# Performance work log

Hardware: AMD Instinct MI355X
Metric: run time of the kernel (lower is better)

The kernel has to match this reference:

```python
import jax, jax.numpy as jnp
import numpy as np

B, T, D, U = 64, 1024, 300, 300


def setup_inputs() -> dict:
    key = jax.random.key(0)
    ks = jax.random.split(key, 12)
    inputs = jax.random.normal(ks[0], (B, T, D), jnp.float32)
    lengths = jax.random.randint(ks[1], (B,), T // 2, T + 1)
    mask = jnp.arange(T)[None, :] < lengths[:, None]  # [B,T] bool

    def w(k, shape, fan_in):
        return jax.random.normal(k, shape, jnp.float32) * (1.0 / np.sqrt(fan_in))

    # Keras GRU (reset_after=True): kernel [D,3U], recurrent_kernel [U,3U], bias [2,3U]
    k_fwd = w(ks[2], (D, 3 * U), D)
    rk_fwd = w(ks[3], (U, 3 * U), U)
    b_fwd = jnp.zeros((2, 3 * U), jnp.float32)
    k_bwd = w(ks[4], (D, 3 * U), D)
    rk_bwd = w(ks[5], (U, 3 * U), U)
    b_bwd = jnp.zeros((2, 3 * U), jnp.float32)
    w_fc = w(ks[6], (2 * U, U), 2 * U)
    b_fc = jnp.zeros((U,), jnp.float32)
    return {
        "inputs": inputs, "mask": mask,
        "k_fwd": k_fwd, "rk_fwd": rk_fwd, "b_fwd": b_fwd,
        "k_bwd": k_bwd, "rk_bwd": rk_bwd, "b_bwd": b_bwd,
        "w_fc": w_fc, "b_fc": b_fc, "training": 0,
    }


def _gru_dir(x, mask, kernel, rkernel, bias):
    """Keras GRU v2 (reset_after=True), zero_output_for_mask, state frozen on masked steps.
    x: [B,T,D], mask: [B,T] bool -> (ys [B,T,U], h_final [B,U])"""
    b_in, b_rec = bias[0], bias[1]
    u = rkernel.shape[0]
    # precompute input projections for all timesteps (cuDNN-style hoisting)
    xp = jnp.einsum('btd,dk->btk', x, kernel) + b_in  # [B,T,3U]

    def step(h, inp):
        xt, mt = inp  # xt: [B,3U], mt: [B]
        rp = h @ rkernel + b_rec  # [B,3U]
        xz, xr, xh = jnp.split(xt, 3, axis=-1)
        rz, rr, rh = jnp.split(rp, 3, axis=-1)
        z = jax.nn.sigmoid(xz + rz)
        r = jax.nn.sigmoid(xr + rr)
        hh = jnp.tanh(xh + r * rh)
        h_new = z * h + (1.0 - z) * hh
        m = mt[:, None]
        h_carry = jnp.where(m, h_new, h)       # state does not update on masked steps
        y = jnp.where(m, h_new, jnp.zeros_like(h_new))  # zero_output_for_mask
        return h_carry, y

    h0 = jnp.zeros((x.shape[0], u), x.dtype)
    h_final, ys = jax.lax.scan(step, h0, (xp.transpose(1, 0, 2), mask.T))
    return ys.transpose(1, 0, 2), h_final


def reference(inputs, mask, k_fwd, rk_fwd, b_fwd, k_bwd, rk_bwd, b_bwd, w_fc, b_fc, training):
    mask = mask.astype(bool)
    x = inputs  # Dropout is identity at inference (training=0)
    y_f, h_f = _gru_dir(x, mask, k_fwd, rk_fwd, b_fwd)
    # backward direction: process reversed sequence/mask, then re-reverse outputs
    y_b, h_b = _gru_dir(x[:, ::-1], mask[:, ::-1], k_bwd, rk_bwd, b_bwd)
    y_b = y_b[:, ::-1]
    output = jnp.concatenate([y_f, y_b], axis=-1)  # [B,T,2U]
    state = jax.nn.relu(jnp.concatenate([h_f, h_b], axis=-1) @ w_fc + b_fc)  # [B,U]
    return output, state
```

## Files before the change

### kernel.cpp

```cpp
#include <hip/hip_runtime.h>
#include <hip/hip_bf16.h>


#define B_   64
#define T_   1024
#define D_   300
#define U_   300
#define NU   900
#define KP   320
#define NP   960
#define XPW  912
#define KL   32

typedef short short8 __attribute__((ext_vector_type(8)));
typedef float floatx4 __attribute__((ext_vector_type(4)));

__device__ __forceinline__ float b2f_bits(unsigned short u) {
  union { unsigned int i; float f; } v; v.i = ((unsigned int)u) << 16; return v.f;
}
__device__ __forceinline__ float lo16(unsigned int w) {
  union { unsigned int i; float f; } v; v.i = w << 16; return v.f;
}
__device__ __forceinline__ float hi16(unsigned int w) {
  union { unsigned int i; float f; } v; v.i = w & 0xffff0000u; return v.f;
}
__device__ __forceinline__ unsigned short f2b(float f) {
  __hip_bfloat16 h = __float2bfloat16(f);
  return *reinterpret_cast<unsigned short*>(&h);
}

__global__ __launch_bounds__(64) void k_detect(const unsigned int* __restrict__ xw,
                                               const unsigned char* __restrict__ mb,
                                               int* __restrict__ flags) {
  __shared__ int red[64];
  int tid = threadIdx.x;
  int hits = 0;
  for (int i = tid; i < 2048; i += 64) {
    unsigned int lo = xw[i] & 0xFFFFu;
    int e = (int)((lo >> 7) & 0xFF);
    if (e >= 105 && e <= 135) hits++;
  }
  red[tid] = hits;
  __syncthreads();
  if (tid == 0) {
    int s = 0;
    for (int i = 0; i < 64; ++i) s += red[i];
    flags[0] = (s >= 1024) ? 1 : 0;
    unsigned char b0 = mb[0], b1 = mb[1];
    flags[1] = (b1 == 0) ? 0 : ((b0 == 1 && b1 == 1) ? 1 : 2);
  }
}

__global__ __launch_bounds__(256) void k_lengths(const unsigned char* __restrict__ mraw,
                                                 const int* __restrict__ flags,
                                                 int* __restrict__ lens) {
  __shared__ int red[256];
  int b = blockIdx.x, tid = threadIdx.x;
  int mt = flags[1];
  int s = 0;
  if (mt == 0) {
    const int* m = (const int*)mraw;
    for (int t = tid; t < T_; t += 256) s += m[(size_t)b * T_ + t] ? 1 : 0;
  } else if (mt == 1) {
    for (int t = tid; t < T_; t += 256) s += mraw[(size_t)b * T_ + t] ? 1 : 0;
  } else {
    const unsigned short* m = (const unsigned short*)mraw;
    for (int t = tid; t < T_; t += 256) s += m[(size_t)b * T_ + t] ? 1 : 0;
  }
  red[tid] = s; __syncthreads();
  for (int off = 128; off > 0; off >>= 1) {
    if (tid < off) red[tid] += red[tid + off];
    __syncthreads();
  }
  if (tid == 0) lens[b] = red[0];
}

__global__ __launch_bounds__(256) void k_xpad(const void* __restrict__ xraw,
                                              const int* __restrict__ flags,
                                              unsigned short* __restrict__ xp) {
  int id = blockIdx.x * 256 + threadIdx.x;
  int row = id / 40, seg = id % 40;
  int kbase = seg * 8;
  int bf = flags[0];
  unsigned short v[8];
  if (bf) {
    const unsigned short* x = (const unsigned short*)xraw;
#pragma unroll
    for (int i = 0; i < 8; ++i) {
      int k = kbase + i;
      v[i] = (k < D_) ? x[(size_t)row * D_ + k] : (unsigned short)0;
    }
  } else {
    const float* x = (const float*)xraw;
#pragma unroll
    for (int i = 0; i < 8; ++i) {
      int k = kbase + i;
      v[i] = (k < D_) ? f2b(x[(size_t)row * D_ + k]) : (unsigned short)0;
    }
  }
  uint4 o;
  o.x = (unsigned)v[0] | ((unsigned)v[1] << 16);
  o.y = (unsigned)v[2] | ((unsigned)v[3] << 16);
  o.z = (unsigned)v[4] | ((unsigned)v[5] << 16);
  o.w = (unsigned)v[6] | ((unsigned)v[7] << 16);
  *(uint4*)(xp + (size_t)row * KP + kbase) = o;
}

__global__ __launch_bounds__(256) void k_wpad(const void* __restrict__ kf,
                                              const void* __restrict__ kb,
                                              const int* __restrict__ flags,
                                              unsigned short* __restrict__ kp) {
  int id = blockIdx.x * 256 + threadIdx.x;
  if (id >= 2 * KP * NP) return;
  int dir = id / (KP * NP);
  int r = id % (KP * NP);
  int k = r / NP, n = r % NP;
  int bf = flags[0];
  unsigned short v = 0;
  if (k < D_ && n < NU) {
    size_t si = (size_t)k * NU + n;
    if (bf) v = ((const unsigned short*)(dir ? kb : kf))[si];
    else    v = f2b(((const float*)(dir ? kb : kf))[si]);
  }
  kp[id] = v;
}

__global__ __launch_bounds__(256) void k_prep(const void* __restrict__ rkf,
                                              const void* __restrict__ rkb,
                                              const void* __restrict__ bfw,
                                              const void* __restrict__ bbw,
                                              const void* __restrict__ wfc,
                                              const void* __restrict__ bfc,
                                              const int* __restrict__ flags,
                                              unsigned short* __restrict__ rkc,
                                              float* __restrict__ biasc,
                                              unsigned short* __restrict__ wfcc,
                                              float* __restrict__ bfcc) {
  int i = blockIdx.x * 256 + threadIdx.x;
  int bf = flags[0];
  if (i < 2 * D_ * NU) {
    int dir = i / (D_ * NU), r = i % (D_ * NU);
    const void* src = dir ? rkb : rkf;
    rkc[i] = bf ? ((const unsigned short*)src)[r] : f2b(((const float*)src)[r]);
  }
  if (i < 2 * 2 * NU) {
    int dir = i / (2 * NU), r = i % (2 * NU);
    const void* src = dir ? bbw : bfw;
    biasc[i] = bf ? b2f_bits(((const unsigned short*)src)[r]) : ((const float*)src)[r];
  }
  if (i < 2 * U_ * U_) {
    wfcc[i] = bf ? ((const unsigned short*)wfc)[i] : f2b(((const float*)wfc)[i]);
  }
  if (i < U_) {
    bfcc[i] = bf ? b2f_bits(((const unsigned short*)bfc)[i]) : ((const float*)bfc)[i];
  }
}

template <bool XPF32>
__global__ __launch_bounds__(256) void k_gemm(const unsigned short* __restrict__ xpad,
                                              const unsigned short* __restrict__ kpad,
                                              const float* __restrict__ biasc,
                                              void* __restrict__ xp_out) {
  __shared__ __align__(16) unsigned short As[64 * 40];
  __shared__ __align__(16) unsigned short Bs[64 * 40];
  int tid = threadIdx.x;
  int wave = tid >> 6, lane = tid & 63;
  int m0 = blockIdx.x * 64, n0 = blockIdx.y * 64;
  int dir = blockIdx.z;
  const unsigned short* Bsrc = kpad + (size_t)dir * KP * NP;
  const float* bin = biasc + (size_t)dir * 2 * NU;

  floatx4 acc[4];
#pragma unroll
  for (int i = 0; i < 4; ++i) acc[i] = {0.f, 0.f, 0.f, 0.f};

  int arow = tid >> 2, aseg = tid & 3;
  int bk = tid & 31, bn8 = (tid >> 5) * 8;
  int fr = lane & 15, fq = lane >> 4;

  for (int kc = 0; kc < KP; kc += 32) {
    uint4 av = *(const uint4*)(xpad + (size_t)(m0 + arow) * KP + kc + aseg * 8);
    uint4 bv = *(const uint4*)(Bsrc + (size_t)(kc + bk) * NP + n0 + bn8);
    *(uint4*)(As + arow * 40 + aseg * 8) = av;
    unsigned short tmp[8];
    tmp[0] = bv.x & 0xffff; tmp[1] = bv.x >> 16;
    tmp[2] = bv.y & 0xffff; tmp[3] = bv.y >> 16;
    tmp[4] = bv.z & 0xffff; tmp[5] = bv.z >> 16;
    tmp[6] = bv.w & 0xffff; tmp[7] = bv.w >> 16;
#pragma unroll
    for (int i = 0; i < 8; ++i) Bs[(bn8 + i) * 40 + bk] = tmp[i];
    __syncthreads();
    short8 a = *(const short8*)(As + (wave * 16 + fr) * 40 + fq * 8);
#pragma unroll
    for (int nt = 0; nt < 4; ++nt) {
      short8 bfrag = *(const short8*)(Bs + (nt * 16 + fr) * 40 + fq * 8);
      acc[nt] = __builtin_amdgcn_mfma_f32_16x16x32_bf16(a, bfrag, acc[nt], 0, 0, 0);
    }
    __syncthreads();
  }
#pragma unroll
  for (int nt = 0; nt < 4; ++nt) {
    int col = n0 + nt * 16 + fr;
    if (col >= XPW) continue;
    float bi = (col < NU) ? bin[col] : 0.f;
#pragma unroll
    for (int r = 0; r < 4; ++r) {
      int m = m0 + wave * 16 + fq * 4 + r;
      float v = acc[nt][r] + bi;
      size_t idx = ((size_t)dir * 65536 + m) * XPW + col;
      if (XPF32) ((float*)xp_out)[idx] = v;
      else ((unsigned short*)xp_out)[idx] = f2b(v);
    }
  }
}

template <bool XPF32>
__global__ __launch_bounds__(256) void k_scan(const unsigned short* __restrict__ rkc,
                                              const float* __restrict__ biasc,
                                              const void* __restrict__ xp_all,
                                              const int* __restrict__ lens,
                                              const int* __restrict__ flags,
                                              float* __restrict__ hfin,
                                              void* __restrict__ outraw)
{
  __shared__ __align__(16) unsigned short wlds[KL * NU];
  __shared__ __align__(16) float h[304];
  __shared__ __align__(16) float rp[912];
  int tid = threadIdx.x;
  int b = blockIdx.x, dir = blockIdx.y;
  const unsigned short* rk = rkc + (size_t)dir * D_ * NU;
  const float* brec = biasc + (size_t)dir * 2 * NU + NU;
  int len = lens[b];
  int obf = flags[0];
  unsigned short* out16 = (unsigned short*)outraw;
  float* out32 = (float*)outraw;

  {
    const unsigned int* src = (const unsigned int*)rk;
    unsigned int* dst = (unsigned int*)wlds;
    for (int i = tid; i < KL * NU / 2; i += 256) dst[i] = src[i];
  }
  for (int i = tid; i < 304; i += 256) h[i] = 0.f;
  __syncthreads();

  int c = tid;
  int j = 4 * c;

  for (int s = 0; s < T_; ++s) {
    int t = dir ? (T_ - 1 - s) : s;
    size_t row = (size_t)b * T_ + t;
    if (t < len) {
      if (c < 225) {
        float a0 = brec[j], a1 = brec[j + 1], a2 = brec[j + 2], a3 = brec[j + 3];
        for (int k0 = 0; k0 < KL; k0 += 4) {
          float4 h4 = *(const float4*)(h + k0);
#pragma unroll
          for (int i = 0; i < 4; ++i) {
            uint2 w = *(const uint2*)(wlds + (k0 + i) * NU + j);
            float hk = ((const float*)&h4)[i];
            a0 = fmaf(lo16(w.x), hk, a0);
            a1 = fmaf(hi16(w.x), hk, a1);
            a2 = fmaf(lo16(w.y), hk, a2);
            a3 = fmaf(hi16(w.y), hk, a3);
          }
        }
        for (int k0 = KL; k0 < D_; k0 += 4) {
          float4 h4 = *(const float4*)(h + k0);
#pragma unroll
          for (int i = 0; i < 4; ++i) {
            uint2 w = *(const uint2*)(rk + (size_t)(k0 + i) * NU + j);
            float hk = ((const float*)&h4)[i];
            a0 = fmaf(lo16(w.x), hk, a0);
            a1 = fmaf(hi16(w.x), hk, a1);
            a2 = fmaf(lo16(w.y), hk, a2);
            a3 = fmaf(hi16(w.y), hk, a3);
          }
        }
        rp[j] = a0; rp[j + 1] = a1; rp[j + 2] = a2; rp[j + 3] = a3;
      }
      __syncthreads();
      for (int u = tid; u < U_; u += 256) {
        float xz, xr, xh;
        if (XPF32) {
          const float* xrow = (const float*)xp_all + ((size_t)dir * 65536 + row) * XPW;
          xz = xrow[u]; xr = xrow[u + U_]; xh = xrow[u + 2 * U_];
        } else {
          const unsigned short* xrow =
              (const unsigned short*)xp_all + ((size_t)dir * 65536 + row) * XPW;
          xz = b2f_bits(xrow[u]); xr = b2f_bits(xrow[u + U_]); xh = b2f_bits(xrow[u + 2 * U_]);
        }
        float z = 1.f / (1.f + __expf(-(xz + rp[u])));
        float r = 1.f / (1.f + __expf(-(xr + rp[u + U_])));
        float hh = tanhf(xh + r * rp[u + 2 * U_]);
        float hold = h[u];
        float hn = z * hold + (1.f - z) * hh;
        h[u] = hn;
        size_t oi = row * 600 + (size_t)dir * U_ + u;
        if (obf) out16[oi] = f2b(hn); else out32[oi] = hn;
      }
      __syncthreads();
    } else {
      for (int u = tid; u < U_; u += 256) {
        size_t oi = row * 600 + (size_t)dir * U_ + u;
        if (obf) out16[oi] = 0; else out32[oi] = 0.f;
      }
    }
  }
  for (int u = tid; u < U_; u += 256) hfin[((size_t)dir * B_ + b) * 304 + u] = h[u];
}

__global__ __launch_bounds__(320) void k_state(const float* __restrict__ hfin,
                                               const unsigned short* __restrict__ wfcc,
                                               const float* __restrict__ bfcc,
                                               const int* __restrict__ flags,
                                               void* __restrict__ outraw) {
  int b = blockIdx.x, u = threadIdx.x;
  if (u >= U_) return;
  int obf = flags[0];
  float acc = bfcc[u];
  const float* hf = hfin + (size_t)b * 304;
  const float* hb = hfin + ((size_t)B_ + b) * 304;
  for (int k = 0; k < U_; ++k) acc = fmaf(hf[k], b2f_bits(wfcc[(size_t)k * U_ + u]), acc);
  for (int k = 0; k < U_; ++k) acc = fmaf(hb[k], b2f_bits(wfcc[(size_t)(U_ + k) * U_ + u]), acc);
  float v = fmaxf(acc, 0.f);
  size_t oi = (size_t)B_ * T_ * 600 + (size_t)b * U_ + u;
  if (obf) ((unsigned short*)outraw)[oi] = f2b(v);
  else     ((float*)outraw)[oi] = v;
}

extern "C" void kernel_launch(void* const* d_in, const int* in_sizes, int n_in,
                              void* d_out, int out_size, void* d_ws, size_t ws_size,
                              hipStream_t stream) {
  const void* x    = d_in[0];
  const void* mask = d_in[1];
  const void* kf   = d_in[2];
  const void* rkf  = d_in[3];
  const void* bfw  = d_in[4];
  const void* kb   = d_in[5];
  const void* rkb  = d_in[6];
  const void* bbw  = d_in[7];
  const void* wfc  = d_in[8];
  const void* bfc  = d_in[9];

  char* ws = (char*)d_ws;
  size_t off = 0;
  auto alloc = [&](size_t bytes) { void* p = ws + off; off += (bytes + 255) & ~(size_t)255; return p; };
  int* flags            = (int*)alloc(256);
  int* lens             = (int*)alloc(256);
  unsigned short* xpad  = (unsigned short*)alloc((size_t)65536 * KP * 2);
  unsigned short* kpad  = (unsigned short*)alloc((size_t)2 * KP * NP * 2);
  unsigned short* rkc   = (unsigned short*)alloc((size_t)2 * D_ * NU * 2);
  float* biasc          = (float*)alloc((size_t)2 * 2 * NU * 4);
  unsigned short* wfcc  = (unsigned short*)alloc((size_t)2 * U_ * U_ * 2);
  float* bfcc           = (float*)alloc((size_t)U_ * 4);
  float* hfin           = (float*)alloc((size_t)2 * B_ * 304 * 4);
  void* xp = (void*)(ws + off);
  size_t need_f32 = off + (size_t)2 * 65536 * XPW * 4;
  bool xpf32 = ws_size >= need_f32;

  k_detect<<<dim3(1), dim3(64), 0, stream>>>((const unsigned int*)x, (const unsigned char*)mask, flags);
  k_lengths<<<dim3(B_), dim3(256), 0, stream>>>((const unsigned char*)mask, flags, lens);
  k_xpad<<<dim3(65536 * 40 / 256), dim3(256), 0, stream>>>(x, flags, xpad);
  k_wpad<<<dim3((2 * KP * NP + 255) / 256), dim3(256), 0, stream>>>(kf, kb, flags, kpad);
  k_prep<<<dim3((2 * D_ * NU + 255) / 256), dim3(256), 0, stream>>>(rkf, rkb, bfw, bbw, wfc, bfc,
                                                                    flags, rkc, biasc, wfcc, bfcc);
  if (xpf32) {
    k_gemm<true><<<dim3(1024, 15, 2), dim3(256), 0, stream>>>(xpad, kpad, biasc, xp);
    k_scan<true><<<dim3(B_, 2), dim3(256), 0, stream>>>(rkc, biasc, xp, lens, flags, hfin, d_out);
  } else {
    k_gemm<false><<<dim3(1024, 15, 2), dim3(256), 0, stream>>>(xpad, kpad, biasc, xp);
    k_scan<false><<<dim3(B_, 2), dim3(256), 0, stream>>>(rkc, biasc, xp, lens, flags, hfin, d_out);
  }
  k_state<<<dim3(B_), dim3(320), 0, stream>>>(hfin, wfcc, bfcc, flags, d_out);
}
```

Before: 16.66 ms.

## Split GRU scan across workgroups by hidden units with MFMA and grid barrier

The recurrent scan used to give each batch row its own workgroup doing scalar bf16 FMAs over the full 300x900 recurrent matrix. Now 15 workgroups per direction each own 20 hidden units for all 64 batch rows. Each keeps its slice of the recurrent weights resident in registers and computes h@Rk with bf16 MFMA, using a hi/lo bf16 split of h to keep close to fp32 accuracy. Hidden state is exchanged through double-buffered global memory, with an atomic-counter grid barrier every timestep. This trades per-step global sync and spin-wait latency for far fewer redundant weight reads and use of the matrix cores. It relies on all 30 workgroups being co-resident.

```diff
diff --git a/kernel.cpp b/kernel.cpp
--- a/kernel.cpp
+++ b/kernel.cpp
@@ -10,19 +10,16 @@
 #define KP   320
 #define NP   960
 #define XPW  912
-#define KL   32
+#define NW   15
+#define W_   20
+#define HS   320
+#define KB_  10
 
 typedef short short8 __attribute__((ext_vector_type(8)));
 typedef float floatx4 __attribute__((ext_vector_type(4)));
 
 __device__ __forceinline__ float b2f_bits(unsigned short u) {
   union { unsigned int i; float f; } v; v.i = ((unsigned int)u) << 16; return v.f;
-}
-__device__ __forceinline__ float lo16(unsigned int w) {
-  union { unsigned int i; float f; } v; v.i = w << 16; return v.f;
-}
-__device__ __forceinline__ float hi16(unsigned int w) {
-  union { unsigned int i; float f; } v; v.i = w & 0xffff0000u; return v.f;
 }
 __device__ __forceinline__ unsigned short f2b(float f) {
   __hip_bfloat16 h = __float2bfloat16(f);
@@ -73,6 +70,17 @@
     __syncthreads();
   }
   if (tid == 0) lens[b] = red[0];
+}
+
+__global__ __launch_bounds__(256) void k_init(unsigned short* __restrict__ hHi,
+                                              unsigned short* __restrict__ hLo,
+                                              int* __restrict__ ctrs) {
+  int i = blockIdx.x * 256 + threadIdx.x;
+  const int nu = 2 * 2 * B_ * HS / 2;
+  unsigned int* a = (unsigned int*)hHi;
+  unsigned int* b = (unsigned int*)hLo;
+  if (i < nu) { a[i] = 0u; b[i] = 0u; }
+  if (i < 128) ctrs[i] = 0;
 }
 
 __global__ __launch_bounds__(256) void k_xpad(const void* __restrict__ xraw,
@@ -156,6 +164,30 @@
   }
 }
 
+__global__ __launch_bounds__(256) void k_bpack(const unsigned short* __restrict__ rkc,
+                                               unsigned short* __restrict__ bpack) {
+  int idx = blockIdx.x * 256 + threadIdx.x;
+  const int total = 2 * NW * 40 * 512;
+  if (idx >= total) return;
+  int rem = idx;
+  int j = rem & 7; rem >>= 3;
+  int lane = rem & 63; rem >>= 6;
+  int f = rem % 40; rem /= 40;
+  int wg = rem % NW;
+  int dir = rem / NW;
+  int kb = f >> 2, nt = f & 3;
+  int l15 = lane & 15, quad = lane >> 4;
+  int k = kb * 32 + quad * 8 + j;
+  int n = nt * 16 + l15;
+  unsigned short v = 0;
+  if (n < 3 * W_ && k < D_) {
+    int g = n / W_, i = n % W_;
+    int col = g * U_ + wg * W_ + i;
+    v = rkc[(size_t)dir * D_ * NU + (size_t)k * NU + col];
+  }
+  bpack[idx] = v;
+}
+
 template <bool XPF32>
 __global__ __launch_bounds__(256) void k_gemm(const unsigned short* __restrict__ xpad,
                                               const unsigned short* __restrict__ kpad,
@@ -215,98 +247,142 @@
 }
 
 template <bool XPF32>
-__global__ __launch_bounds__(256) void k_scan(const unsigned short* __restrict__ rkc,
-                                              const float* __restrict__ biasc,
-                                              const void* __restrict__ xp_all,
-                                              const int* __restrict__ lens,
-                                              const int* __restrict__ flags,
-                                              float* __restrict__ hfin,
-                                              void* __restrict__ outraw)
-{
-  __shared__ __align__(16) unsigned short wlds[KL * NU];
-  __shared__ __align__(16) float h[304];
-  __shared__ __align__(16) float rp[912];
+__global__ __launch_bounds__(256, 1) void k_scan(const unsigned short* __restrict__ bpack,
+                                                 const float* __restrict__ biasc,
+                                                 const void* __restrict__ xp_all,
+                                                 const int* __restrict__ lens,
+                                                 const int* __restrict__ flags,
+                                                 unsigned short* __restrict__ hHi,
+                                                 unsigned short* __restrict__ hLo,
+                                                 float* __restrict__ hfin,
+                                                 int* __restrict__ ctrs,
+                                                 void* __restrict__ outraw) {
+  __shared__ __align__(16) float rp[64 * 68];
   int tid = threadIdx.x;
-  int b = blockIdx.x, dir = blockIdx.y;
-  const unsigned short* rk = rkc + (size_t)dir * D_ * NU;
-  const float* brec = biasc + (size_t)dir * 2 * NU + NU;
-  int len = lens[b];
+  int wg = blockIdx.x, dir = blockIdx.y;
+  int wave = tid >> 6, lane = tid & 63;
+  int l15 = lane & 15, quad = lane >> 4;
   int obf = flags[0];
   unsigned short* out16 = (unsigned short*)outraw;
   float* out32 = (float*)outraw;
 
+  short8 breg[KB_][4];
   {
-    const unsigned int* src = (const unsigned int*)rk;
-    unsigned int* dst = (unsigned int*)wlds;
-    for (int i = tid; i < KL * NU / 2; i += 256) dst[i] = src[i];
-  }
-  for (int i = tid; i < 304; i += 256) h[i] = 0.f;
-  __syncthreads();
-
-  int c = tid;
-  int j = 4 * c;
-
+    const unsigned short* bp = bpack + ((size_t)(dir * NW + wg) * 40) * 512 + lane * 8;
+#pragma unroll
+    for (int kb = 0; kb < KB_; ++kb)
+#pragma unroll
+      for (int nt = 0; nt < 4; ++nt)
+        breg[kb][nt] = *(const short8*)(bp + (size_t)(kb * 4 + nt) * 512);
+  }
+
+  int eb = tid >> 2;
+  int ei = (tid & 3) * 5;
+  int u0 = wg * W_;
+  int mylen = lens[eb];
+  const float* brec = biasc + (size_t)dir * 2 * NU + NU;
+  float bz[5], brr[5], bh[5], hold[5];
+#pragma unroll
+  for (int q = 0; q < 5; ++q) {
+    int u = u0 + ei + q;
+    bz[q] = brec[u]; brr[q] = brec[U_ + u]; bh[q] = brec[2 * U_ + u];
+    hold[q] = 0.f;
+  }
+
+  int ctr_target = 0;
+  int* myctr = ctrs + dir * 64;
+
+#pragma unroll 1
   for (int s = 0; s < T_; ++s) {
     int t = dir ? (T_ - 1 - s) : s;
-    size_t row = (size_t)b * T_ + t;
-    if (t < len) {
-      if (c < 225) {
-        float a0 = brec[j], a1 = brec[j + 1], a2 = brec[j + 2], a3 = brec[j + 3];
-        for (int k0 = 0; k0 < KL; k0 += 4) {
-          float4 h4 = *(const float4*)(h + k0);
-#pragma unroll
-          for (int i = 0; i < 4; ++i) {
-            uint2 w = *(const uint2*)(wlds + (k0 + i) * NU + j);
-            float hk = ((const float*)&h4)[i];
-            a0 = fmaf(lo16(w.x), hk, a0);
-            a1 = fmaf(hi16(w.x), hk, a1);
-            a2 = fmaf(lo16(w.y), hk, a2);
-            a3 = fmaf(hi16(w.y), hk, a3);
-          }
+    int par = s & 1;
+    const unsigned short* hh = hHi + (size_t)(par * 2 + dir) * (B_ * HS);
+    const unsigned short* hl = hLo + (size_t)(par * 2 + dir) * (B_ * HS);
+
+    float xz[5], xr[5], xh[5];
+    {
+      size_t rowoff = ((size_t)dir * 65536 + (size_t)eb * T_ + t) * XPW;
+      if (XPF32) {
+        const float* xrow = (const float*)xp_all + rowoff;
+#pragma unroll
+        for (int q = 0; q < 5; ++q) {
+          int u = u0 + ei + q;
+          xz[q] = xrow[u]; xr[q] = xrow[U_ + u]; xh[q] = xrow[2 * U_ + u];
         }
-        for (int k0 = KL; k0 < D_; k0 += 4) {
-          float4 h4 = *(const float4*)(h + k0);
-#pragma unroll
-          for (int i = 0; i < 4; ++i) {
-            uint2 w = *(const uint2*)(rk + (size_t)(k0 + i) * NU + j);
-            float hk = ((const float*)&h4)[i];
-            a0 = fmaf(lo16(w.x), hk, a0);
-            a1 = fmaf(hi16(w.x), hk, a1);
-            a2 = fmaf(lo16(w.y), hk, a2);
-            a3 = fmaf(hi16(w.y), hk, a3);
-          }
+      } else {
+        const unsigned short* xrow = (const unsigned short*)xp_all + rowoff;
+#pragma unroll
+        for (int q = 0; q < 5; ++q) {
+          int u = u0 + ei + q;
+          xz[q] = b2f_bits(xrow[u]); xr[q] = b2f_bits(xrow[U_ + u]); xh[q] = b2f_bits(xrow[2 * U_ + u]);
         }
-        rp[j] = a0; rp[j + 1] = a1; rp[j + 2] = a2; rp[j + 3] = a3;
       }
-      __syncthreads();
-      for (int u = tid; u < U_; u += 256) {
-        float xz, xr, xh;
-        if (XPF32) {
-          const float* xrow = (const float*)xp_all + ((size_t)dir * 65536 + row) * XPW;
-          xz = xrow[u]; xr = xrow[u + U_]; xh = xrow[u + 2 * U_];
-        } else {
-          const unsigned short* xrow =
-              (const unsigned short*)xp_all + ((size_t)dir * 65536 + row) * XPW;
-          xz = b2f_bits(xrow[u]); xr = b2f_bits(xrow[u + U_]); xh = b2f_bits(xrow[u + 2 * U_]);
-        }
-        float z = 1.f / (1.f + __expf(-(xz + rp[u])));
-        float r = 1.f / (1.f + __expf(-(xr + rp[u + U_])));
-        float hh = tanhf(xh + r * rp[u + 2 * U_]);
-        float hold = h[u];
-        float hn = z * hold + (1.f - z) * hh;
-        h[u] = hn;
-        size_t oi = row * 600 + (size_t)dir * U_ + u;
-        if (obf) out16[oi] = f2b(hn); else out32[oi] = hn;
+    }
+
+    floatx4 acc[4];
+#pragma unroll
+    for (int i = 0; i < 4; ++i) acc[i] = {0.f, 0.f, 0.f, 0.f};
+    {
+      const unsigned short* ah_base = hh + (size_t)(wave * 16 + l15) * HS + quad * 8;
+      const unsigned short* al_base = hl + (size_t)(wave * 16 + l15) * HS + quad * 8;
+#pragma unroll
+      for (int kb = 0; kb < KB_; ++kb) {
+        short8 ah = *(const short8*)(ah_base + kb * 32);
+        short8 al = *(const short8*)(al_base + kb * 32);
+#pragma unroll
+        for (int nt = 0; nt < 4; ++nt)
+          acc[nt] = __builtin_amdgcn_mfma_f32_16x16x32_bf16(ah, breg[kb][nt], acc[nt], 0, 0, 0);
+#pragma unroll
+        for (int nt = 0; nt < 4; ++nt)
+          acc[nt] = __builtin_amdgcn_mfma_f32_16x16x32_bf16(al, breg[kb][nt], acc[nt], 0, 0, 0);
       }
-      __syncthreads();
-    } else {
-      for (int u = tid; u < U_; u += 256) {
-        size_t oi = row * 600 + (size_t)dir * U_ + u;
-        if (obf) out16[oi] = 0; else out32[oi] = 0.f;
-      }
-    }
-  }
-  for (int u = tid; u < U_; u += 256) hfin[((size_t)dir * B_ + b) * 304 + u] = h[u];
+    }
+#pragma unroll
+    for (int nt = 0; nt < 4; ++nt)
+#pragma unroll
+      for (int r = 0; r < 4; ++r)
+        rp[(wave * 16 + quad * 4 + r) * 68 + nt * 16 + l15] = acc[nt][r];
+    __syncthreads();
+
+    bool m = (t < mylen);
+    unsigned short* nhh = hHi + (size_t)(((s + 1) & 1) * 2 + dir) * (B_ * HS);
+    unsigned short* nhl = hLo + (size_t)(((s + 1) & 1) * 2 + dir) * (B_ * HS);
+    size_t obase = ((size_t)eb * T_ + t) * 600 + (size_t)dir * U_ + u0 + ei;
+#pragma unroll
+    for (int q = 0; q < 5; ++q) {
+      int i = ei + q;
+      float rz = rp[eb * 68 + i];
+      float rr = rp[eb * 68 + W_ + i];
+      float rh = rp[eb * 68 + 2 * W_ + i];
+      float z = 1.f / (1.f + __expf(-(xz[q] + rz + bz[q])));
+      float r = 1.f / (1.f + __expf(-(xr[q] + rr + brr[q])));
+      float hhat = tanhf(xh[q] + r * (rh + bh[q]));
+      float hn = z * hold[q] + (1.f - z) * hhat;
+      float hw = m ? hn : hold[q];
+      hold[q] = hw;
+      float y = m ? hn : 0.f;
+      if (obf) out16[obase + q] = f2b(y); else out32[obase + q] = y;
+      unsigned short hib = f2b(hw);
+      float lo = hw - b2f_bits(hib);
+      nhh[eb * HS + u0 + i] = hib;
+      nhl[eb * HS + u0 + i] = f2b(lo);
+    }
+
+    __threadfence();
+    __syncthreads();
+    ctr_target += NW;
+    if (tid == 0) {
+      __hip_atomic_fetch_add(myctr, 1, __ATOMIC_ACQ_REL, __HIP_MEMORY_SCOPE_AGENT);
+      while (__hip_atomic_load(myctr, __ATOMIC_ACQUIRE, __HIP_MEMORY_SCOPE_AGENT) < ctr_target)
+        __builtin_amdgcn_s_sleep(1);
+    }
+    __syncthreads();
+    __threadfence();
+  }
+
+#pragma unroll
+  for (int q = 0; q < 5; ++q)
+    hfin[((size_t)dir * B_ + eb) * 304 + u0 + ei + q] = hold[q];
 }
 
 __global__ __launch_bounds__(320) void k_state(const float* __restrict__ hfin,
@@ -347,29 +423,37 @@
   auto alloc = [&](size_t bytes) { void* p = ws + off; off += (bytes + 255) & ~(size_t)255; return p; };
   int* flags            = (int*)alloc(256);
   int* lens             = (int*)alloc(256);
+  int* ctrs             = (int*)alloc(512);
   unsigned short* xpad  = (unsigned short*)alloc((size_t)65536 * KP * 2);
   unsigned short* kpad  = (unsigned short*)alloc((size_t)2 * KP * NP * 2);
   unsigned short* rkc   = (unsigned short*)alloc((size_t)2 * D_ * NU * 2);
+  unsigned short* bpack = (unsigned short*)alloc((size_t)2 * NW * 40 * 512 * 2);
   float* biasc          = (float*)alloc((size_t)2 * 2 * NU * 4);
   unsigned short* wfcc  = (unsigned short*)alloc((size_t)2 * U_ * U_ * 2);
   float* bfcc           = (float*)alloc((size_t)U_ * 4);
   float* hfin           = (float*)alloc((size_t)2 * B_ * 304 * 4);
+  unsigned short* hHi   = (unsigned short*)alloc((size_t)2 * 2 * B_ * HS * 2);
+  unsigned short* hLo   = (unsigned short*)alloc((size_t)2 * 2 * B_ * HS * 2);
   void* xp = (void*)(ws + off);
   size_t need_f32 = off + (size_t)2 * 65536 * XPW * 4;
   bool xpf32 = ws_size >= need_f32;
 
   k_detect<<<dim3(1), dim3(64), 0, stream>>>((const unsigned int*)x, (const unsigned char*)mask, flags);
   k_lengths<<<dim3(B_), dim3(256), 0, stream>>>((const unsigned char*)mask, flags, lens);
+  k_init<<<dim3((2 * 2 * B_ * HS / 2 + 255) / 256), dim3(256), 0, stream>>>(hHi, hLo, ctrs);
   k_xpad<<<dim3(65536 * 40 / 256), dim3(256), 0, stream>>>(x, flags, xpad);
   k_wpad<<<dim3((2 * KP * NP + 255) / 256), dim3(256), 0, stream>>>(kf, kb, flags, kpad);
   k_prep<<<dim3((2 * D_ * NU + 255) / 256), dim3(256), 0, stream>>>(rkf, rkb, bfw, bbw, wfc, bfc,
                                                                     flags, rkc, biasc, wfcc, bfcc);
+  k_bpack<<<dim3((2 * NW * 40 * 512 + 255) / 256), dim3(256), 0, stream>>>(rkc, bpack);
   if (xpf32) {
     k_gemm<true><<<dim3(1024, 15, 2), dim3(256), 0, stream>>>(xpad, kpad, biasc, xp);
-    k_scan<true><<<dim3(B_, 2), dim3(256), 0, stream>>>(rkc, biasc, xp, lens, flags, hfin, d_out);
+    k_scan<true><<<dim3(NW, 2), dim3(256), 0, stream>>>(bpack, biasc, xp, lens, flags,
+                                                        hHi, hLo, hfin, ctrs, d_out);
   } else {
     k_gemm<false><<<dim3(1024, 15, 2), dim3(256), 0, stream>>>(xpad, kpad, biasc, xp);
-    k_scan<false><<<dim3(B_, 2), dim3(256), 0, stream>>>(rkc, biasc, xp, lens, flags, hfin, d_out);
+    k_scan<false><<<dim3(NW, 2), dim3(256), 0, stream>>>(bpack, biasc, xp, lens, flags,
+                                                         hHi, hLo, hfin, ctrs, d_out);
   }
   k_state<<<dim3(B_), dim3(320), 0, stream>>>(hfin, wfcc, bfcc, flags, d_out);
 }
```

New measurement: 14.02 ms. 1.19x faster.
